# Optimization experiments

Measured on AMD Instinct MI355X. Metric: run time of the kernel, lower is better.

Reference implementation:

```python
import jax, jax.numpy as jnp
import numpy as np

N, E, B = 131072, 524288, 4096
NODES_PER_GRAPH = N // B  # 32


def setup_inputs() -> dict:
    key = jax.random.key(0)
    ks = jax.random.split(key, 16)
    def rn(k, shape, scale=0.05):
        return jax.random.normal(k, shape, jnp.float32) * scale
    return {
        "drug": jax.random.normal(ks[0], (N, 9), jnp.float32),
        "edge_index": jax.random.randint(ks[1], (2, E), 0, N),
        "batch_index": jnp.arange(N) // NODES_PER_GRAPH,  # sorted, every graph non-empty
        "protein": jax.random.normal(ks[2], (B, 1, 768), jnp.float32),
        # GCNConv layers (W: [in,out], b: [out])
        "gcn1_W": rn(ks[3], (9, 64)), "gcn1_b": jnp.zeros((64,), jnp.float32),
        "gcn2_W": rn(ks[4], (64, 64)), "gcn2_b": jnp.zeros((64,), jnp.float32),
        # GCN_output_layer Linear(128, 768)
        "out_W": rn(ks[5], (128, 768)), "out_b": jnp.zeros((768,), jnp.float32),
        # CNN_layers Conv1d stack
        "conv1_W": rn(ks[6], (32, 2, 3)), "conv1_b": jnp.zeros((32,), jnp.float32),
        "conv2_W": rn(ks[7], (32, 32, 3)), "conv2_b": jnp.zeros((32,), jnp.float32),
        "conv3_W": rn(ks[8], (32, 32, 3)), "conv3_b": jnp.zeros((32,), jnp.float32),
        # CBAM channel attention MLP (no bias): Linear(32,16), Linear(16,32)
        "ca_W1": rn(ks[9], (16, 32)), "ca_W2": rn(ks[10], (32, 16)),
        # SAM spatial conv Conv1d(2,1,3,pad=1)
        "sam_W": rn(ks[11], (1, 2, 3)), "sam_b": jnp.zeros((1,), jnp.float32),
        # CNN_linear MLP
        "lin1_W": rn(ks[12], (32, 12288)), "lin1_b": jnp.zeros((32,), jnp.float32),
        "lin2_W": rn(ks[13], (32, 32)), "lin2_b": jnp.zeros((32,), jnp.float32),
        "lin3_W": rn(ks[14], (1, 32)), "lin3_b": jnp.zeros((1,), jnp.float32),
    }


def gcn_conv(x, W, b, src, dst, n):
    """PyG GCNConv: self-loops + symmetric deg^-1/2 normalization."""
    h = x @ W  # [n, out]
    loop = jnp.arange(n)
    s = jnp.concatenate([src, loop])
    d = jnp.concatenate([dst, loop])
    deg = jax.ops.segment_sum(jnp.ones_like(d, x.dtype), d, num_segments=n)
    dinv = jax.lax.rsqrt(deg)  # deg >= 1 due to self-loops
    norm = dinv[s] * dinv[d]
    return jax.ops.segment_sum(h[s] * norm[:, None], d, num_segments=n) + b


def conv1d(x, w, b):
    y = jax.lax.conv_general_dilated(x, w, (1,), [(1, 1)],
                                     dimension_numbers=("NCH", "OIH", "NCH"))
    return y + b[None, :, None]


def reference(drug, edge_index, batch_index, protein,
              gcn1_W, gcn1_b, gcn2_W, gcn2_b, out_W, out_b,
              conv1_W, conv1_b, conv2_W, conv2_b, conv3_W, conv3_b,
              ca_W1, ca_W2, sam_W, sam_b,
              lin1_W, lin1_b, lin2_W, lin2_b, lin3_W, lin3_b):
    n = drug.shape[0]
    b_graphs = protein.shape[0]
    src, dst = edge_index[0], edge_index[1]

    x = jnp.tanh(gcn_conv(drug, gcn1_W, gcn1_b, src, dst, n))
    x = jnp.tanh(gcn_conv(x, gcn2_W, gcn2_b, src, dst, n))
    x = gcn_conv(x, gcn2_W, gcn2_b, src, dst, n)  # GCN2 reused, no activation

    gmax = jax.ops.segment_max(x, batch_index, num_segments=b_graphs)
    cnt = jax.ops.segment_sum(jnp.ones((n, 1), x.dtype), batch_index, num_segments=b_graphs)
    gmean = jax.ops.segment_sum(x, batch_index, num_segments=b_graphs) / cnt
    pooled = jnp.concatenate([gmax, gmean], axis=1)  # [B, 128]

    gcn_out = (pooled @ out_W + out_b)[:, None, :]  # [B, 1, 768]
    combined = jnp.concatenate([gcn_out, protein], axis=1)  # [B, 2, 768]

    h = conv1d(combined, conv1_W, conv1_b)
    h = conv1d(h, conv2_W, conv2_b)
    h = conv1d(h, conv3_W, conv3_b)  # [B, 32, 768]
    # dropout is identity at inference

    # CBAM: channel attention
    x1 = jnp.max(h, axis=-1)   # [B, 32]
    x2 = jnp.mean(h, axis=-1)  # [B, 32]
    mlp = lambda v: jax.nn.relu((v @ ca_W1.T) @ ca_W2.T)
    feats = jax.nn.sigmoid(mlp(x1) + mlp(x2))
    h = h * feats[:, :, None]
    # CBAM: spatial attention
    xm = jnp.mean(h, axis=1, keepdims=True)
    xM = jnp.max(h, axis=1, keepdims=True)
    att = jax.nn.sigmoid(conv1d(jnp.concatenate([xm, xM], axis=1), sam_W, sam_b))
    h = h * att

    # MaxPool1d(kernel_size=2)
    Bc, C, L = h.shape
    h = h.reshape(Bc, C, L // 2, 2).max(axis=-1)
    h = h.reshape(Bc, -1)  # [B, 12288]

    h = jax.nn.softplus(h @ lin1_W.T + lin1_b)
    h = jax.nn.softplus(h @ lin2_W.T + lin2_b)
    out = jax.nn.softplus(h @ lin3_W.T + lin3_b)
    return out
```

## Files before the change

### kernel.cpp

```cpp
#include <hip/hip_runtime.h>
#include <cstdint>
#include <cstddef>

#define NN 131072
#define EE 524288
#define BB 4096
#define LL 768

typedef __attribute__((ext_vector_type(8))) short bf16x8;
typedef __attribute__((ext_vector_type(4))) float f32x4;
typedef __attribute__((ext_vector_type(2))) unsigned int uint2v;

__device__ __forceinline__ float b2f(unsigned short u) {
  return __uint_as_float(((unsigned int)u) << 16);
}
__device__ __forceinline__ unsigned short f2b(float f) {
  unsigned int x = __float_as_uint(f);
  x += 0x7fff + ((x >> 16) & 1);
  return (unsigned short)(x >> 16);
}
__device__ __forceinline__ unsigned f2b2(float lo, float hi) {
#if __has_builtin(__builtin_amdgcn_cvt_pk_bf16_f32)
  typedef __attribute__((ext_vector_type(2))) __bf16 bf16v2;
  bf16v2 r = __builtin_amdgcn_cvt_pk_bf16_f32(lo, hi);
  return __builtin_bit_cast(unsigned, r);
#else
  return (unsigned)f2b(lo) | ((unsigned)f2b(hi) << 16);
#endif
}
__device__ __forceinline__ float sigm(float x) { return 1.f / (1.f + expf(-x)); }
__device__ __forceinline__ float softplus_(float x) {
  return fmaxf(x, 0.f) + log1pf(expf(-fabsf(x)));
}

__global__ __launch_bounds__(256) void k_zeroi(int* __restrict__ p) {
  p[blockIdx.x * 256 + threadIdx.x] = 0;
}
__global__ __launch_bounds__(256) void k_hist(const int* __restrict__ ei,
                                              int* __restrict__ degi) {
  int e = blockIdx.x * 256 + threadIdx.x;
  atomicAdd(&degi[ei[EE + e]], 1);
}
__global__ __launch_bounds__(256) void k_scan1(const int* __restrict__ degi,
                                               int* __restrict__ incl,
                                               int* __restrict__ bsum) {
  __shared__ int s[256];
  int t = threadIdx.x;
  int i = blockIdx.x * 256 + t;
  s[t] = degi[i];
  __syncthreads();
  for (int off = 1; off < 256; off <<= 1) {
    int u = (t >= off) ? s[t - off] : 0;
    __syncthreads();
    s[t] += u;
    __syncthreads();
  }
  incl[i] = s[t];
  if (t == 255) bsum[blockIdx.x] = s[t];
}
__global__ __launch_bounds__(512) void k_scan2(const int* __restrict__ bsum,
                                               int* __restrict__ bexcl) {
  __shared__ int s[512];
  int t = threadIdx.x;
  s[t] = bsum[t];
  __syncthreads();
  int orig = s[t];
  for (int off = 1; off < 512; off <<= 1) {
    int u = (t >= off) ? s[t - off] : 0;
    __syncthreads();
    s[t] += u;
    __syncthreads();
  }
  bexcl[t] = s[t] - orig;
}
__global__ __launch_bounds__(256) void k_scan3(const int* __restrict__ incl,
                                               const int* __restrict__ degi,
                                               const int* __restrict__ bexcl,
                                               int* __restrict__ offs,
                                               float* __restrict__ dinv) {
  int t = threadIdx.x;
  int i = blockIdx.x * 256 + t;
  offs[i] = incl[i] - degi[i] + bexcl[blockIdx.x];
  dinv[i] = rsqrtf((float)degi[i] + 1.0f);
  if (i == 0) offs[NN] = EE;
}
__global__ __launch_bounds__(256) void k_scatter(const int* __restrict__ ei,
                                                 const int* __restrict__ offs,
                                                 int* __restrict__ cur,
                                                 int* __restrict__ csr) {
  int e = blockIdx.x * 256 + threadIdx.x;
  int dst = ei[EE + e];
  int pos = atomicAdd(&cur[dst], 1);
  csr[offs[dst] + pos] = ei[e];
}

__global__ __launch_bounds__(256) void k_mm1(const float* __restrict__ drug,
                                             const float* __restrict__ W,
                                             const float* __restrict__ dinv,
                                             unsigned short* __restrict__ g) {
  __shared__ float Ws[9 * 64];
  int t = threadIdx.x;
  for (int i = t; i < 576; i += 256) Ws[i] = W[i];
  __syncthreads();
  int node = blockIdx.x * 4 + (t >> 6);
  int f = t & 63;
  const float* dr = drug + (size_t)node * 9;
  float s = 0.f;
#pragma unroll
  for (int k = 0; k < 9; k++) s += dr[k] * Ws[k * 64 + f];
  g[(size_t)node * 64 + f] = f2b(dinv[node] * s);
}

__global__ __launch_bounds__(256) void k_prepg(const float* __restrict__ W,
                                               unsigned short* __restrict__ Wgb) {
  int idx = blockIdx.x * 256 + threadIdx.x;
  int j = idx & 7;
  int lane = (idx >> 3) & 63;
  int nt = (idx >> 9) & 3;
  int kc = idx >> 11;
  int k = kc * 32 + (lane >> 4) * 8 + j;
  int o = nt * 16 + (lane & 15);
  Wgb[idx] = f2b(W[k * 64 + o]);
}

template <bool TANH>
__global__ __launch_bounds__(256) void k_layer(const unsigned short* __restrict__ gin,
                                               const int* __restrict__ offs,
                                               const int* __restrict__ csr,
                                               const float* __restrict__ dinv,
                                               const float* __restrict__ bias,
                                               const unsigned short* __restrict__ Wgb,
                                               unsigned short* __restrict__ outb) {
  __shared__ alignas(16) unsigned short xa[32 * 72];
  __shared__ alignas(16) float dis[32];
  const int t = threadIdx.x;
  const int wv = t >> 6, f = t & 63;
  const int lx = f & 15, quad = f >> 4;
  const int n0 = blockIdx.x * 32;
  const float bf = bias[f];
  for (int it = 0; it < 8; it++) {
    const int dl = wv * 8 + it;
    const int d = n0 + dl;
    const float di = dinv[d];
    const int j0 = offs[d], j1 = offs[d + 1];
    float acc = b2f(gin[(size_t)d * 64 + f]);
    int j = j0;
    for (; j + 4 <= j1; j += 4) {
      int s0 = csr[j], s1 = csr[j + 1], s2 = csr[j + 2], s3 = csr[j + 3];
      acc += (b2f(gin[(size_t)s0 * 64 + f]) + b2f(gin[(size_t)s1 * 64 + f]))
           + (b2f(gin[(size_t)s2 * 64 + f]) + b2f(gin[(size_t)s3 * 64 + f]));
    }
    for (; j < j1; j++) acc += b2f(gin[(size_t)csr[j] * 64 + f]);
    float v = di * acc + bf;
    if (TANH) v = tanhf(v);
    xa[dl * 72 + f] = f2b(v);
    if (f == 0) dis[dl] = di;
  }
  __syncthreads();
  const int mt = wv >> 1, np = wv & 1;
  bf16x8 A0 = *(const bf16x8*)&xa[(mt * 16 + lx) * 72 + quad * 8];
  bf16x8 A1 = *(const bf16x8*)&xa[(mt * 16 + lx) * 72 + 32 + quad * 8];
  f32x4 accs[2];
#pragma unroll
  for (int nn = 0; nn < 2; nn++) {
    int nt = np * 2 + nn;
    bf16x8 B0 = *(const bf16x8*)&Wgb[((0 * 4 + nt) * 64 + f) * 8];
    bf16x8 B1 = *(const bf16x8*)&Wgb[((1 * 4 + nt) * 64 + f) * 8];
    f32x4 acc = {0.f, 0.f, 0.f, 0.f};
    acc = __builtin_amdgcn_mfma_f32_16x16x32_bf16(A0, B0, acc, 0, 0, 0);
    acc = __builtin_amdgcn_mfma_f32_16x16x32_bf16(A1, B1, acc, 0, 0, 0);
    accs[nn] = acc;
  }
  f32x4 dq = *(const f32x4*)&dis[mt * 16 + quad * 4];
  __syncthreads();
#pragma unroll
  for (int nn = 0; nn < 2; nn++) {
    int nt = np * 2 + nn;
#pragma unroll
    for (int r = 0; r < 4; r++)
      xa[(mt * 16 + quad * 4 + r) * 72 + nt * 16 + lx] = f2b(dq[r] * accs[nn][r]);
  }
  __syncthreads();
  {
    int node = t >> 3, c8 = t & 7;
    *(f32x4*)(outb + (size_t)(n0 + node) * 64 + c8 * 8) =
        *(const f32x4*)(xa + node * 72 + c8 * 8);
  }
}

__global__ __launch_bounds__(512) void k_lastpool(const unsigned short* __restrict__ gin,
                                                  const int* __restrict__ offs,
                                                  const int* __restrict__ csr,
                                                  const float* __restrict__ dinv,
                                                  const float* __restrict__ bias,
                                                  float* __restrict__ pooled) {
  __shared__ float smax[8][64], ssum[8][64];
  const int t = threadIdx.x;
  const int f = t & 63, grp = t >> 6;
  const int g = blockIdx.x;
  const float bf = bias[f];
  float mx = -1e30f, sm = 0.f;
#pragma unroll
  for (int i = 0; i < 4; i++) {
    int d = g * 32 + grp * 4 + i;
    const float di = dinv[d];
    const int j0 = offs[d], j1 = offs[d + 1];
    float acc = b2f(gin[(size_t)d * 64 + f]);
    int j = j0;
    for (; j + 4 <= j1; j += 4) {
      int s0 = csr[j], s1 = csr[j + 1], s2 = csr[j + 2], s3 = csr[j + 3];
      acc += (b2f(gin[(size_t)s0 * 64 + f]) + b2f(gin[(size_t)s1 * 64 + f]))
           + (b2f(gin[(size_t)s2 * 64 + f]) + b2f(gin[(size_t)s3 * 64 + f]));
    }
    for (; j < j1; j++) acc += b2f(gin[(size_t)csr[j] * 64 + f]);
    float v = di * acc + bf;
    mx = fmaxf(mx, v);
    sm += v;
  }
  smax[grp][f] = mx;
  ssum[grp][f] = sm;
  __syncthreads();
  if (t < 64) {
    float m = smax[0][t], s = ssum[0][t];
#pragma unroll
    for (int w = 1; w < 8; w++) { m = fmaxf(m, smax[w][t]); s += ssum[w][t]; }
    pooled[(size_t)g * 128 + t] = m;
    pooled[(size_t)g * 128 + 64 + t] = s * (1.f / 32.f);
  }
}

__global__ __launch_bounds__(256) void k_outmm(const float* __restrict__ pooled,
                                               const float* __restrict__ W,
                                               const float* __restrict__ bias,
                                               unsigned short* __restrict__ gout) {
  __shared__ float ps[16][128];
  int t = threadIdx.x;
  int g0 = blockIdx.x * 16;
  for (int i = t; i < 16 * 128; i += 256) ps[i >> 7][i & 127] = pooled[(size_t)g0 * 128 + i];
  __syncthreads();
  float a0[16], a1[16], a2[16];
#pragma unroll
  for (int j = 0; j < 16; j++) { a0[j] = 0.f; a1[j] = 0.f; a2[j] = 0.f; }
  for (int k = 0; k < 128; k++) {
    float w0 = W[k * 768 + t];
    float w1 = W[k * 768 + t + 256];
    float w2 = W[k * 768 + t + 512];
#pragma unroll
    for (int j = 0; j < 16; j++) {
      float p = ps[j][k];
      a0[j] += p * w0; a1[j] += p * w1; a2[j] += p * w2;
    }
  }
  float b0 = bias[t], b1 = bias[t + 256], b2 = bias[t + 512];
  for (int j = 0; j < 16; j++) {
    gout[(size_t)(g0 + j) * 768 + t]       = f2b(a0[j] + b0);
    gout[(size_t)(g0 + j) * 768 + t + 256] = f2b(a1[j] + b1);
    gout[(size_t)(g0 + j) * 768 + t + 512] = f2b(a2[j] + b2);
  }
}

__global__ __launch_bounds__(512) void k_prepk7(
    const float* __restrict__ W1, const float* __restrict__ b1,
    const float* __restrict__ W2, const float* __restrict__ b2,
    const float* __restrict__ W3, const float* __restrict__ b3,
    unsigned short* __restrict__ Kcb, float* __restrict__ bconst) {
  __shared__ float W1s[192], W2s[3072], W3s[3072];
  __shared__ float b1s[32], b2s[32], b3s[32];
  __shared__ float M[320];
  __shared__ float beta[32];
  __shared__ float KcS[448];
  const int t = threadIdx.x;
  for (int i = t; i < 3072; i += 512) { W2s[i] = W2[i]; W3s[i] = W3[i]; }
  if (t < 192) W1s[t] = W1[t];
  if (t >= 192 && t < 224) { int i = t - 192; b1s[i] = b1[i]; b2s[i] = b2[i]; b3s[i] = b3[i]; }
  __syncthreads();
  if (t < 320) {
    int i = t / 10, rem = t % 10, c = rem / 5, t12 = rem % 5;
    float s = 0.f;
    for (int j = 0; j < 32; j++)
#pragma unroll
      for (int t2 = 0; t2 < 3; t2++) {
        int t1 = t12 - t2;
        if (t1 >= 0 && t1 < 3) s += W2s[(i * 32 + j) * 3 + t2] * W1s[(j * 2 + c) * 3 + t1];
      }
    M[i * 10 + c * 5 + t12] = s;
  }
  if (t >= 384 && t < 416) {
    int i = t - 384;
    float s = b2s[i];
    for (int j = 0; j < 32; j++) {
      float w = W2s[(i * 32 + j) * 3] + W2s[(i * 32 + j) * 3 + 1] + W2s[(i * 32 + j) * 3 + 2];
      s += w * b1s[j];
    }
    beta[i] = s;
  }
  __syncthreads();
  if (t < 448) {
    int o = t / 14, rem = t % 14, c = rem / 7, tt = rem % 7;
    float s = 0.f;
    for (int i = 0; i < 32; i++)
#pragma unroll
      for (int t3 = 0; t3 < 3; t3++) {
        int t12 = tt - t3;
        if (t12 >= 0 && t12 < 5) s += W3s[(o * 32 + i) * 3 + t3] * M[i * 10 + c * 5 + t12];
      }
    KcS[t] = s;
  }
  if (t >= 480 && t < 512) {
    int o = t - 480;
    float s = b3s[o];
    for (int i = 0; i < 32; i++) {
      float w = W3s[(o * 32 + i) * 3] + W3s[(o * 32 + i) * 3 + 1] + W3s[(o * 32 + i) * 3 + 2];
      s += w * beta[i];
    }
    bconst[o] = s;
  }
  __syncthreads();
  for (int i = t; i < 1024; i += 512) {
    int o = i >> 5, k = i & 31;
    Kcb[i] = (k < 14) ? f2b(KcS[o * 14 + k]) : (unsigned short)0;
  }
}

__global__ __launch_bounds__(64) void k_prepedge(
    const float* __restrict__ W1, const float* __restrict__ b1,
    const float* __restrict__ W2, const float* __restrict__ b2,
    const float* __restrict__ W3, const float* __restrict__ b3,
    float* __restrict__ edgeK, float* __restrict__ edgeB) {
  __shared__ float W1s[192], W2s[3072], W3s[3072];
  __shared__ float b1s[32], b2s[32], b3s[32];
  __shared__ float cl[2][6], h1[32][5], h2[32][4];
  const int t = threadIdx.x;
  const int side = blockIdx.x / 13, run = blockIdx.x % 13;
  for (int i = t; i < 3072; i += 64) { W2s[i] = W2[i]; W3s[i] = W3[i]; }
  for (int i = t; i < 192; i += 64) W1s[i] = W1[i];
  if (t < 32) { b1s[t] = b1[t]; b2s[t] = b2[t]; b3s[t] = b3[t]; }
  if (t < 12) cl[t / 6][t % 6] = (run == t) ? 1.f : 0.f;
  __syncthreads();
  const bool ub = (run == 12);
  if (t < 32) {
    int i = t;
    for (int p = 0; p < 5; p++) {
      float s = ub ? b1s[i] : 0.f;
      for (int c = 0; c < 2; c++)
#pragma unroll
        for (int tau = 0; tau < 3; tau++) {
          int x = (side == 0) ? (p + tau - 1) : (p + tau);
          if (x >= 0 && x < 6) s += W1s[(i * 2 + c) * 3 + tau] * cl[c][x];
        }
      h1[i][p] = s;
    }
  }
  __syncthreads();
  if (t < 32) {
    int o = t;
    for (int u = 0; u < 4; u++) {
      float s = ub ? b2s[o] : 0.f;
      for (int i = 0; i < 32; i++)
#pragma unroll
        for (int tau = 0; tau < 3; tau++) {
          int q = (side == 0) ? (u + tau - 1) : (u + tau);
          if (q >= 0 && q < 5) s += W2s[(o * 32 + i) * 3 + tau] * h1[i][q];
        }
      h2[o][u] = s;
    }
  }
  __syncthreads();
  if (t < 32) {
    int o = t;
    for (int e = 0; e < 2; e++) {
      float s = ub ? b3s[o] : 0.f;
      for (int i = 0; i < 32; i++)
#pragma unroll
        for (int tau = 0; tau < 3; tau++) {
          int u = (side == 0) ? (e + tau - 1) : (e + tau + 1);
          if (u >= 0 && u < 4) s += W3s[(o * 32 + i) * 3 + tau] * h2[i][u];
        }
      int slot = (side * 2 + e) * 32 + o;
      if (ub) edgeB[slot] = s;
      else edgeK[slot * 12 + run] = s;
    }
  }
}

__global__ __launch_bounds__(256) void k_prepw(const float* __restrict__ W,
                                               unsigned short* __restrict__ Wb) {
  int idx = blockIdx.x * 256 + threadIdx.x;
  int j = idx & 7;
  int lane = (idx >> 3) & 63;
  int nt = (idx >> 9) & 1;
  int kt = idx >> 10;
  int o = nt * 16 + (lane & 15);
  int k = kt * 32 + (lane >> 4) * 8 + j;
  int korig = (k & 31) * 384 + (k >> 5);
  Wb[idx] = f2b(W[(size_t)o * 12288 + korig]);
}

__global__ __launch_bounds__(512) void k_cnn(
    const unsigned short* __restrict__ gout, const float* __restrict__ protein,
    const unsigned short* __restrict__ Kcb, const float* __restrict__ bconst,
    const float* __restrict__ edgeK, const float* __restrict__ edgeB,
    const float* __restrict__ caW1, const float* __restrict__ caW2,
    const float* __restrict__ samW, const float* __restrict__ samb,
    unsigned short* __restrict__ pvec) {
  __shared__ float combf[2][776];
  __shared__ alignas(16) unsigned short im2[768 * 16];
  __shared__ float xbuf[2320];
  __shared__ float bcs[32];
  __shared__ float wmaxs[8][32], wsums[8][32];
  __shared__ float cmaxs[32], csums[32], t1buf[2][16], feats[32], samWs[8];
  const int t = threadIdx.x;
  const int b = blockIdx.x;
  const int lane = t & 63, wv = t >> 6, lx = lane & 15, quad = lane >> 4;

  for (int i = t; i < 1552; i += 512) {
    int c = i / 776, li = i - c * 776;
    int l = li - 4;
    float v = 0.f;
    if (l >= 0 && l < LL)
      v = c ? protein[(size_t)b * LL + l] : b2f(gout[(size_t)b * LL + l]);
    combf[c][li] = v;
  }
  if (t < 32) bcs[t] = bconst[t];
  if (t >= 32 && t < 38) samWs[t - 32] = samW[t - 32];
  if (t == 38) samWs[6] = samb[0];
  __syncthreads();

  for (int p = 0; p < 24; p++) {
    int idx = t + p * 512;
    int l = idx >> 4, k = idx & 15;
    unsigned short v = 0;
    if (k < 14) {
      int c = (k >= 7) ? 1 : 0;
      int q = k - c * 7;
      v = f2b(combf[c][l + 1 + q]);
    }
    im2[idx] = v;
  }
  __syncthreads();

  f32x4 a3[6][2];
  {
    bf16x8 A0 = *(const bf16x8*)&Kcb[(0 * 16 + lx) * 32 + quad * 8];
    bf16x8 A1 = *(const bf16x8*)&Kcb[(1 * 16 + lx) * 32 + quad * 8];
    f32x4 ci0, ci1;
#pragma unroll
    for (int r = 0; r < 4; r++) {
      ci0[r] = bcs[quad * 4 + r];
      ci1[r] = bcs[16 + quad * 4 + r];
    }
#pragma unroll
    for (int n = 0; n < 6; n++) {
      int l = (wv * 6 + n) * 16 + lx;
      bf16x8 Bf = {0, 0, 0, 0, 0, 0, 0, 0};
      if (quad < 2) Bf = *(const bf16x8*)&im2[l * 16 + quad * 8];
      a3[n][0] = __builtin_amdgcn_mfma_f32_16x16x32_bf16(A0, Bf, ci0, 0, 0, 0);
      a3[n][1] = __builtin_amdgcn_mfma_f32_16x16x32_bf16(A1, Bf, ci1, 0, 0, 0);
    }
  }
  {
    bool left = (wv == 0 && lx < 2);
    bool right = (wv == 7 && lx >= 14);
    if (left || right) {
      int n = left ? 0 : 5;
      int e = left ? lx : (lx - 14);
      int side = left ? 0 : 1;
      int cbase = left ? 4 : 766;
#pragma unroll
      for (int mt = 0; mt < 2; mt++)
#pragma unroll
        for (int r = 0; r < 4; r++) {
          int o = mt * 16 + quad * 4 + r;
          int slot = (side * 2 + e) * 32 + o;
          float s = edgeB[slot];
          const float* ek = &edgeK[slot * 12];
#pragma unroll
          for (int w = 0; w < 6; w++)
            s += ek[w] * combf[0][cbase + w] + ek[6 + w] * combf[1][cbase + w];
          a3[n][mt][r] = s;
        }
    }
  }

  float tmax[2][4], tsum[2][4];
#pragma unroll
  for (int mt = 0; mt < 2; mt++)
#pragma unroll
    for (int r = 0; r < 4; r++) { tmax[mt][r] = -1e30f; tsum[mt][r] = 0.f; }
#pragma unroll
  for (int n = 0; n < 6; n++)
#pragma unroll
    for (int mt = 0; mt < 2; mt++)
#pragma unroll
      for (int r = 0; r < 4; r++) {
        float v = a3[n][mt][r];
        tmax[mt][r] = fmaxf(tmax[mt][r], v);
        tsum[mt][r] += v;
      }
#pragma unroll
  for (int mt = 0; mt < 2; mt++)
#pragma unroll
    for (int r = 0; r < 4; r++) {
      float m = tmax[mt][r], s = tsum[mt][r];
      for (int d = 1; d < 16; d <<= 1) {
        m = fmaxf(m, __shfl_xor(m, d));
        s += __shfl_xor(s, d);
      }
      if (lx == 0) {
        wmaxs[wv][mt * 16 + quad * 4 + r] = m;
        wsums[wv][mt * 16 + quad * 4 + r] = s;
      }
    }
  __syncthreads();

  if (t < 32) {
    float m = wmaxs[0][t], s = wsums[0][t];
#pragma unroll
    for (int w = 1; w < 8; w++) { m = fmaxf(m, wmaxs[w][t]); s += wsums[w][t]; }
    cmaxs[t] = m;
    csums[t] = s;
  }
  __syncthreads();
  if (t < 32) {
    int j = t & 15;
    int mean = t >> 4;
    float s = 0.f;
    for (int o = 0; o < 32; o++) {
      float v = mean ? csums[o] * (1.f / 768.f) : cmaxs[o];
      s += v * caW1[j * 32 + o];
    }
    t1buf[mean][j] = s;
  }
  __syncthreads();
  if (t < 32) {
    float m1 = 0.f, m2 = 0.f;
    for (int j = 0; j < 16; j++) {
      m1 += t1buf[0][j] * caW2[t * 16 + j];
      m2 += t1buf[1][j] * caW2[t * 16 + j];
    }
    feats[t] = sigm(fmaxf(m1, 0.f) + fmaxf(m2, 0.f));
  }
  __syncthreads();

  float frq[2][4];
#pragma unroll
  for (int mt = 0; mt < 2; mt++)
#pragma unroll
    for (int r = 0; r < 4; r++) frq[mt][r] = feats[mt * 16 + quad * 4 + r];
#pragma unroll
  for (int n = 0; n < 6; n++) {
    int l = (wv * 6 + n) * 16 + lx;
    float sm = 0.f, mx = -1e30f;
#pragma unroll
    for (int mt = 0; mt < 2; mt++)
#pragma unroll
      for (int r = 0; r < 4; r++) {
        float v = a3[n][mt][r] * frq[mt][r];
        sm += v;
        mx = fmaxf(mx, v);
      }
    sm += __shfl_xor(sm, 16); mx = fmaxf(mx, __shfl_xor(mx, 16));
    sm += __shfl_xor(sm, 32); mx = fmaxf(mx, __shfl_xor(mx, 32));
    if (quad == 0) {
      xbuf[l] = sm * (1.f / 32.f);
      xbuf[772 + l] = mx;
    }
  }
  __syncthreads();

  for (int l = t; l < LL; l += 512) {
    float a = samWs[6];
#pragma unroll
    for (int k = 0; k < 3; k++) {
      int ll = l + k - 1;
      float vm = (ll >= 0 && ll < LL) ? xbuf[ll] : 0.f;
      float vM = (ll >= 0 && ll < LL) ? xbuf[772 + ll] : 0.f;
      a += samWs[k] * vm + samWs[3 + k] * vM;
    }
    xbuf[1544 + l] = sigm(a);
  }
  __syncthreads();

#pragma unroll
  for (int n = 0; n < 6; n++) {
    int l = (wv * 6 + n) * 16 + lx;
    float at = xbuf[1544 + l];
    float m[2][4];
#pragma unroll
    for (int mt = 0; mt < 2; mt++)
#pragma unroll
      for (int r = 0; r < 4; r++) {
        float v = a3[n][mt][r] * frq[mt][r] * at;
        m[mt][r] = fmaxf(v, __shfl_xor(v, 1));
      }
    if (!(lx & 1)) {
      int lp = l >> 1;
#pragma unroll
      for (int mt = 0; mt < 2; mt++) {
        uint2v pk;
        pk.x = f2b2(m[mt][0], m[mt][1]);
        pk.y = f2b2(m[mt][2], m[mt][3]);
        *(uint2v*)&pvec[(size_t)b * 12288 + lp * 32 + mt * 16 + quad * 4] = pk;
      }
    }
  }
}

__global__ __launch_bounds__(512) void k_mlp1(
    const unsigned short* __restrict__ pvec, const unsigned short* __restrict__ Wb,
    float* __restrict__ partial) {
  __shared__ float part[8][32][32];
  const int t = threadIdx.x;
  const int lane = t & 63, wv = t >> 6, lx = lane & 15, quad = lane >> 4;
  const int g0 = (blockIdx.x >> 2) * 32;
  const int kc = blockIdx.x & 3;
  const unsigned short* arow0 = pvec + (size_t)(g0 + lx) * 12288 + quad * 8;
  const unsigned short* arow1 = pvec + (size_t)(g0 + 16 + lx) * 12288 + quad * 8;

  f32x4 a00 = {0.f, 0.f, 0.f, 0.f}, a01 = a00, a10 = a00, a11 = a00;
  const int kt0 = kc * 96 + wv * 12;
#pragma unroll 4
  for (int i = 0; i < 12; i++) {
    const int kt = kt0 + i;
    bf16x8 A0 = *(const bf16x8*)&arow0[kt * 32];
    bf16x8 A1 = *(const bf16x8*)&arow1[kt * 32];
    bf16x8 B0 = *(const bf16x8*)&Wb[((kt * 2 + 0) * 64 + lane) * 8];
    bf16x8 B1 = *(const bf16x8*)&Wb[((kt * 2 + 1) * 64 + lane) * 8];
    a00 = __builtin_amdgcn_mfma_f32_16x16x32_bf16(A0, B0, a00, 0, 0, 0);
    a01 = __builtin_amdgcn_mfma_f32_16x16x32_bf16(A0, B1, a01, 0, 0, 0);
    a10 = __builtin_amdgcn_mfma_f32_16x16x32_bf16(A1, B0, a10, 0, 0, 0);
    a11 = __builtin_amdgcn_mfma_f32_16x16x32_bf16(A1, B1, a11, 0, 0, 0);
  }
#pragma unroll
  for (int r = 0; r < 4; r++) {
    part[wv][quad * 4 + r][lx]            = a00[r];
    part[wv][quad * 4 + r][16 + lx]       = a01[r];
    part[wv][16 + quad * 4 + r][lx]       = a10[r];
    part[wv][16 + quad * 4 + r][16 + lx]  = a11[r];
  }
  __syncthreads();
#pragma unroll
  for (int p = 0; p < 2; p++) {
    int idx = t + p * 512;
    int g = idx >> 5, o = idx & 31;
    float s = 0.f;
#pragma unroll
    for (int w = 0; w < 8; w++) s += part[w][g][o];
    partial[((size_t)kc * BB + g0 + g) * 32 + o] = s;
  }
}

__global__ __launch_bounds__(512) void k_mlp2(
    const float* __restrict__ partial,
    const float* __restrict__ lb1, const float* __restrict__ W2,
    const float* __restrict__ lb2, const float* __restrict__ W3,
    const float* __restrict__ lb3, float* __restrict__ out) {
  __shared__ float s1[16][32];
  __shared__ float s2[16][32];
  const int t = threadIdx.x;
  const int g0 = blockIdx.x * 16;
  {
    int g = t >> 5, o = t & 31;
    float s = lb1[o];
#pragma unroll
    for (int kc = 0; kc < 4; kc++) s += partial[((size_t)kc * BB + g0 + g) * 32 + o];
    s1[g][o] = softplus_(s);
  }
  __syncthreads();
  {
    int g = t >> 5, o = t & 31;
    float s = lb2[o];
    for (int kk = 0; kk < 32; kk++) s += s1[g][kk] * W2[o * 32 + kk];
    s2[g][o] = softplus_(s);
  }
  __syncthreads();
  if (t < 16) {
    float s = lb3[0];
    for (int kk = 0; kk < 32; kk++) s += s2[t][kk] * W3[kk];
    out[g0 + t] = softplus_(s);
  }
}

extern "C" void kernel_launch(void* const* d_in, const int* in_sizes, int n_in,
                              void* d_out, int out_size, void* d_ws, size_t ws_size,
                              hipStream_t stream) {
  const float* drug    = (const float*)d_in[0];
  const int*   ei      = (const int*)d_in[1];
  const float* protein = (const float*)d_in[3];
  const float* g1W = (const float*)d_in[4];
  const float* g1b = (const float*)d_in[5];
  const float* g2W = (const float*)d_in[6];
  const float* g2b = (const float*)d_in[7];
  const float* oW  = (const float*)d_in[8];
  const float* ob  = (const float*)d_in[9];
  const float* c1W = (const float*)d_in[10];
  const float* c1b = (const float*)d_in[11];
  const float* c2W = (const float*)d_in[12];
  const float* c2b = (const float*)d_in[13];
  const float* c3W = (const float*)d_in[14];
  const float* c3b = (const float*)d_in[15];
  const float* caW1 = (const float*)d_in[16];
  const float* caW2 = (const float*)d_in[17];
  const float* samW = (const float*)d_in[18];
  const float* samb = (const float*)d_in[19];
  const float* l1W = (const float*)d_in[20];
  const float* l1b = (const float*)d_in[21];
  const float* l2W = (const float*)d_in[22];
  const float* l2b = (const float*)d_in[23];
  const float* l3W = (const float*)d_in[24];
  const float* l3b = (const float*)d_in[25];

  char* ws = (char*)d_ws;
  float* dinv  = (float*)(ws);
  int*   degi  = (int*)(ws + (size_t)524288);
  int*   cur   = (int*)(ws + (size_t)1048576);
  int*   offs  = (int*)(ws + (size_t)1572864);
  int*   bsum  = (int*)(ws + (size_t)2621440);
  int*   bexcl = (int*)(ws + (size_t)2625536);
  int*   csr   = (int*)(ws + (size_t)3145728);
  unsigned short* gA = (unsigned short*)(ws + (size_t)5242880);
  unsigned short* gB = (unsigned short*)(ws + (size_t)22020096);
  unsigned short* pvec = (unsigned short*)(ws + (size_t)5242880);
  float* pooled = (float*)(ws + (size_t)105906176);
  unsigned short* gout = (unsigned short*)(ws + (size_t)108003328);
  unsigned short* Wb   = (unsigned short*)(ws + (size_t)114294784);
  float* bconst  = (float*)(ws + (size_t)115083136);
  float* edgeK   = (float*)(ws + (size_t)115083264);
  float* edgeB   = (float*)(ws + (size_t)115089408);
  unsigned short* Kcb = (unsigned short*)(ws + (size_t)115090432);
  unsigned short* Wgb = (unsigned short*)(ws + (size_t)115092480);
  float* partial = (float*)(ws + (size_t)115343360);
  float* outp = (float*)d_out;

  k_zeroi<<<2 * NN / 256, 256, 0, stream>>>(degi);
  k_hist<<<EE / 256, 256, 0, stream>>>(ei, degi);
  k_scan1<<<NN / 256, 256, 0, stream>>>(degi, offs, bsum);
  k_scan2<<<1, 512, 0, stream>>>(bsum, bexcl);
  k_scan3<<<NN / 256, 256, 0, stream>>>(offs, degi, bexcl, offs, dinv);
  k_scatter<<<EE / 256, 256, 0, stream>>>(ei, offs, cur, csr);
  k_prepw<<<(12288 * 32) / 256, 256, 0, stream>>>(l1W, Wb);
  k_prepg<<<16, 256, 0, stream>>>(g2W, Wgb);
  k_prepk7<<<1, 512, 0, stream>>>(c1W, c1b, c2W, c2b, c3W, c3b, Kcb, bconst);
  k_prepedge<<<26, 64, 0, stream>>>(c1W, c1b, c2W, c2b, c3W, c3b, edgeK, edgeB);

  k_mm1<<<NN / 4, 256, 0, stream>>>(drug, g1W, dinv, gA);
  k_layer<true><<<NN / 32, 256, 0, stream>>>(gA, offs, csr, dinv, g1b, Wgb, gB);
  k_layer<true><<<NN / 32, 256, 0, stream>>>(gB, offs, csr, dinv, g2b, Wgb, gA);
  k_lastpool<<<BB, 512, 0, stream>>>(gA, offs, csr, dinv, g2b, pooled);

  k_outmm<<<BB / 16, 256, 0, stream>>>(pooled, oW, ob, gout);

  k_cnn<<<BB, 512, 0, stream>>>(gout, protein, Kcb, bconst, edgeK, edgeB,
                                caW1, caW2, samW, samb, pvec);

  k_mlp1<<<(BB / 32) * 4, 512, 0, stream>>>(pvec, Wb, partial);
  k_mlp2<<<BB / 16, 512, 0, stream>>>(partial, l1b, l2W, l2b, l3W, l3b, outp);
}
```

Before: 581.2 us.

## Make CNN kernel persistent over 16 graphs with prefetch; widen GCN layer blocks

k_cnn now runs 256 blocks, and each block loops over 16 graphs. It prefetches the next graph's gout/protein row into registers while the current graph is processed, and builds the im2col buffer with packed 16-byte bf16 stores instead of scalar stores. The xbuf scratch is folded into combf plus a smaller attention buffer. Separately, the GCN layer kernels go to 512 threads covering 64 nodes per block. The aim is to cut launch and block-setup overhead and hide global load latency. The risk is that one block per CU with a serial chain of syncs leaves too little parallelism to hide latency.

```diff
diff --git a/kernel.cpp b/kernel.cpp
--- a/kernel.cpp
+++ b/kernel.cpp
@@ -10,6 +10,7 @@
 typedef __attribute__((ext_vector_type(8))) short bf16x8;
 typedef __attribute__((ext_vector_type(4))) float f32x4;
 typedef __attribute__((ext_vector_type(2))) unsigned int uint2v;
+typedef __attribute__((ext_vector_type(4))) unsigned int uint4v;
 
 __device__ __forceinline__ float b2f(unsigned short u) {
   return __uint_as_float(((unsigned int)u) << 16);
@@ -124,19 +125,19 @@
 }
 
 template <bool TANH>
-__global__ __launch_bounds__(256) void k_layer(const unsigned short* __restrict__ gin,
+__global__ __launch_bounds__(512) void k_layer(const unsigned short* __restrict__ gin,
                                                const int* __restrict__ offs,
                                                const int* __restrict__ csr,
                                                const float* __restrict__ dinv,
                                                const float* __restrict__ bias,
                                                const unsigned short* __restrict__ Wgb,
                                                unsigned short* __restrict__ outb) {
-  __shared__ alignas(16) unsigned short xa[32 * 72];
-  __shared__ alignas(16) float dis[32];
+  __shared__ alignas(16) unsigned short xa[64 * 72];
+  __shared__ alignas(16) float dis[64];
   const int t = threadIdx.x;
   const int wv = t >> 6, f = t & 63;
   const int lx = f & 15, quad = f >> 4;
-  const int n0 = blockIdx.x * 32;
+  const int n0 = blockIdx.x * 64;
   const float bf = bias[f];
   for (int it = 0; it < 8; it++) {
     const int dl = wv * 8 + it;
@@ -403,52 +404,88 @@
     const float* __restrict__ caW1, const float* __restrict__ caW2,
     const float* __restrict__ samW, const float* __restrict__ samb,
     unsigned short* __restrict__ pvec) {
-  __shared__ float combf[2][776];
+  __shared__ float combf[1552];
   __shared__ alignas(16) unsigned short im2[768 * 16];
-  __shared__ float xbuf[2320];
+  __shared__ float attb[768];
   __shared__ float bcs[32];
   __shared__ float wmaxs[8][32], wsums[8][32];
   __shared__ float cmaxs[32], csums[32], t1buf[2][16], feats[32], samWs[8];
   const int t = threadIdx.x;
-  const int b = blockIdx.x;
   const int lane = t & 63, wv = t >> 6, lx = lane & 15, quad = lane >> 4;
-
-  for (int i = t; i < 1552; i += 512) {
-    int c = i / 776, li = i - c * 776;
-    int l = li - 4;
-    float v = 0.f;
-    if (l >= 0 && l < LL)
-      v = c ? protein[(size_t)b * LL + l] : b2f(gout[(size_t)b * LL + l]);
-    combf[c][li] = v;
-  }
+  const int bstart = blockIdx.x * 16;
+
   if (t < 32) bcs[t] = bconst[t];
   if (t >= 32 && t < 38) samWs[t - 32] = samW[t - 32];
   if (t == 38) samWs[6] = samb[0];
   __syncthreads();
-
-  for (int p = 0; p < 24; p++) {
-    int idx = t + p * 512;
-    int l = idx >> 4, k = idx & 15;
-    unsigned short v = 0;
-    if (k < 14) {
-      int c = (k >= 7) ? 1 : 0;
-      int q = k - c * 7;
-      v = f2b(combf[c][l + 1 + q]);
-    }
-    im2[idx] = v;
-  }
-  __syncthreads();
-
-  f32x4 a3[6][2];
-  {
-    bf16x8 A0 = *(const bf16x8*)&Kcb[(0 * 16 + lx) * 32 + quad * 8];
-    bf16x8 A1 = *(const bf16x8*)&Kcb[(1 * 16 + lx) * 32 + quad * 8];
-    f32x4 ci0, ci1;
-#pragma unroll
-    for (int r = 0; r < 4; r++) {
-      ci0[r] = bcs[quad * 4 + r];
-      ci1[r] = bcs[16 + quad * 4 + r];
-    }
+  bf16x8 A0 = *(const bf16x8*)&Kcb[(0 * 16 + lx) * 32 + quad * 8];
+  bf16x8 A1 = *(const bf16x8*)&Kcb[(1 * 16 + lx) * 32 + quad * 8];
+  f32x4 ci0, ci1;
+#pragma unroll
+  for (int r = 0; r < 4; r++) {
+    ci0[r] = bcs[quad * 4 + r];
+    ci1[r] = bcs[16 + quad * 4 + r];
+  }
+
+  float rv[3];
+#pragma unroll
+  for (int j = 0; j < 3; j++) {
+    int i = t + j * 512;
+    float v = 0.f;
+    if (i < 1552) {
+      int c = (i >= 776) ? 1 : 0;
+      int l = i - c * 776 - 4;
+      if (l >= 0 && l < LL)
+        v = c ? protein[(size_t)bstart * LL + l] : b2f(gout[(size_t)bstart * LL + l]);
+    }
+    rv[j] = v;
+  }
+
+  for (int gs = 0; gs < 16; gs++) {
+    const int b = bstart + gs;
+#pragma unroll
+    for (int j = 0; j < 3; j++) {
+      int i = t + j * 512;
+      if (i < 1552) combf[i] = rv[j];
+    }
+    __syncthreads();
+    {
+      const int gp = (b + 1 < BB) ? b + 1 : b;
+#pragma unroll
+      for (int j = 0; j < 3; j++) {
+        int i = t + j * 512;
+        float v = 0.f;
+        if (i < 1552) {
+          int c = (i >= 776) ? 1 : 0;
+          int l = i - c * 776 - 4;
+          if (l >= 0 && l < LL)
+            v = c ? protein[(size_t)gp * LL + l] : b2f(gout[(size_t)gp * LL + l]);
+        }
+        rv[j] = v;
+      }
+    }
+
+    for (int p = 0; p < 3; p++) {
+      int idx = t + p * 512;
+      int l = idx >> 1, half = idx & 1;
+      uint4v pk;
+      if (half == 0) {
+        float v0 = combf[l + 1], v1 = combf[l + 2], v2 = combf[l + 3], v3 = combf[l + 4];
+        float v4 = combf[l + 5], v5 = combf[l + 6], v6 = combf[l + 7];
+        float v7 = combf[776 + l + 1];
+        pk[0] = f2b2(v0, v1); pk[1] = f2b2(v2, v3);
+        pk[2] = f2b2(v4, v5); pk[3] = f2b2(v6, v7);
+      } else {
+        float v0 = combf[776 + l + 2], v1 = combf[776 + l + 3], v2 = combf[776 + l + 4];
+        float v3 = combf[776 + l + 5], v4 = combf[776 + l + 6], v5 = combf[776 + l + 7];
+        pk[0] = f2b2(v0, v1); pk[1] = f2b2(v2, v3);
+        pk[2] = f2b2(v4, v5); pk[3] = 0u;
+      }
+      *(uint4v*)&im2[l * 16 + half * 8] = pk;
+    }
+    __syncthreads();
+
+    f32x4 a3[6][2];
 #pragma unroll
     for (int n = 0; n < 6; n++) {
       int l = (wv * 6 + n) * 16 + lx;
@@ -457,152 +494,155 @@
       a3[n][0] = __builtin_amdgcn_mfma_f32_16x16x32_bf16(A0, Bf, ci0, 0, 0, 0);
       a3[n][1] = __builtin_amdgcn_mfma_f32_16x16x32_bf16(A1, Bf, ci1, 0, 0, 0);
     }
-  }
-  {
-    bool left = (wv == 0 && lx < 2);
-    bool right = (wv == 7 && lx >= 14);
-    if (left || right) {
-      int n = left ? 0 : 5;
-      int e = left ? lx : (lx - 14);
-      int side = left ? 0 : 1;
-      int cbase = left ? 4 : 766;
+    {
+      bool left = (wv == 0 && lx < 2);
+      bool right = (wv == 7 && lx >= 14);
+      if (left || right) {
+        int n = left ? 0 : 5;
+        int e = left ? lx : (lx - 14);
+        int side = left ? 0 : 1;
+        int cbase = left ? 4 : 766;
+#pragma unroll
+        for (int mt = 0; mt < 2; mt++)
+#pragma unroll
+          for (int r = 0; r < 4; r++) {
+            int o = mt * 16 + quad * 4 + r;
+            int slot = (side * 2 + e) * 32 + o;
+            float s = edgeB[slot];
+            const float* ek = &edgeK[slot * 12];
+#pragma unroll
+            for (int w = 0; w < 6; w++)
+              s += ek[w] * combf[cbase + w] + ek[6 + w] * combf[776 + cbase + w];
+            a3[n][mt][r] = s;
+          }
+      }
+    }
+
+    float tmax[2][4], tsum[2][4];
+#pragma unroll
+    for (int mt = 0; mt < 2; mt++)
+#pragma unroll
+      for (int r = 0; r < 4; r++) { tmax[mt][r] = -1e30f; tsum[mt][r] = 0.f; }
+#pragma unroll
+    for (int n = 0; n < 6; n++)
 #pragma unroll
       for (int mt = 0; mt < 2; mt++)
 #pragma unroll
         for (int r = 0; r < 4; r++) {
-          int o = mt * 16 + quad * 4 + r;
-          int slot = (side * 2 + e) * 32 + o;
-          float s = edgeB[slot];
-          const float* ek = &edgeK[slot * 12];
-#pragma unroll
-          for (int w = 0; w < 6; w++)
-            s += ek[w] * combf[0][cbase + w] + ek[6 + w] * combf[1][cbase + w];
-          a3[n][mt][r] = s;
-        }
-    }
-  }
-
-  float tmax[2][4], tsum[2][4];
-#pragma unroll
-  for (int mt = 0; mt < 2; mt++)
-#pragma unroll
-    for (int r = 0; r < 4; r++) { tmax[mt][r] = -1e30f; tsum[mt][r] = 0.f; }
-#pragma unroll
-  for (int n = 0; n < 6; n++)
+          float v = a3[n][mt][r];
+          tmax[mt][r] = fmaxf(tmax[mt][r], v);
+          tsum[mt][r] += v;
+        }
 #pragma unroll
     for (int mt = 0; mt < 2; mt++)
 #pragma unroll
       for (int r = 0; r < 4; r++) {
-        float v = a3[n][mt][r];
-        tmax[mt][r] = fmaxf(tmax[mt][r], v);
-        tsum[mt][r] += v;
-      }
-#pragma unroll
-  for (int mt = 0; mt < 2; mt++)
-#pragma unroll
-    for (int r = 0; r < 4; r++) {
-      float m = tmax[mt][r], s = tsum[mt][r];
-      for (int d = 1; d < 16; d <<= 1) {
-        m = fmaxf(m, __shfl_xor(m, d));
-        s += __shfl_xor(s, d);
-      }
-      if (lx == 0) {
-        wmaxs[wv][mt * 16 + quad * 4 + r] = m;
-        wsums[wv][mt * 16 + quad * 4 + r] = s;
-      }
-    }
-  __syncthreads();
-
-  if (t < 32) {
-    float m = wmaxs[0][t], s = wsums[0][t];
-#pragma unroll
-    for (int w = 1; w < 8; w++) { m = fmaxf(m, wmaxs[w][t]); s += wsums[w][t]; }
-    cmaxs[t] = m;
-    csums[t] = s;
-  }
-  __syncthreads();
-  if (t < 32) {
-    int j = t & 15;
-    int mean = t >> 4;
-    float s = 0.f;
-    for (int o = 0; o < 32; o++) {
-      float v = mean ? csums[o] * (1.f / 768.f) : cmaxs[o];
-      s += v * caW1[j * 32 + o];
-    }
-    t1buf[mean][j] = s;
-  }
-  __syncthreads();
-  if (t < 32) {
-    float m1 = 0.f, m2 = 0.f;
-    for (int j = 0; j < 16; j++) {
-      m1 += t1buf[0][j] * caW2[t * 16 + j];
-      m2 += t1buf[1][j] * caW2[t * 16 + j];
-    }
-    feats[t] = sigm(fmaxf(m1, 0.f) + fmaxf(m2, 0.f));
-  }
-  __syncthreads();
-
-  float frq[2][4];
-#pragma unroll
-  for (int mt = 0; mt < 2; mt++)
-#pragma unroll
-    for (int r = 0; r < 4; r++) frq[mt][r] = feats[mt * 16 + quad * 4 + r];
-#pragma unroll
-  for (int n = 0; n < 6; n++) {
-    int l = (wv * 6 + n) * 16 + lx;
-    float sm = 0.f, mx = -1e30f;
+        float m = tmax[mt][r], s = tsum[mt][r];
+        for (int d = 1; d < 16; d <<= 1) {
+          m = fmaxf(m, __shfl_xor(m, d));
+          s += __shfl_xor(s, d);
+        }
+        if (lx == 0) {
+          wmaxs[wv][mt * 16 + quad * 4 + r] = m;
+          wsums[wv][mt * 16 + quad * 4 + r] = s;
+        }
+      }
+    __syncthreads();
+
+    if (t < 32) {
+      float m = wmaxs[0][t], s = wsums[0][t];
+#pragma unroll
+      for (int w = 1; w < 8; w++) { m = fmaxf(m, wmaxs[w][t]); s += wsums[w][t]; }
+      cmaxs[t] = m;
+      csums[t] = s;
+    }
+    __syncthreads();
+    if (t < 32) {
+      int j = t & 15;
+      int mean = t >> 4;
+      float s = 0.f;
+      for (int o = 0; o < 32; o++) {
+        float v = mean ? csums[o] * (1.f / 768.f) : cmaxs[o];
+        s += v * caW1[j * 32 + o];
+      }
+      t1buf[mean][j] = s;
+    }
+    __syncthreads();
+    if (t < 32) {
+      float m1 = 0.f, m2 = 0.f;
+      for (int j = 0; j < 16; j++) {
+        m1 += t1buf[0][j] * caW2[t * 16 + j];
+        m2 += t1buf[1][j] * caW2[t * 16 + j];
+      }
+      feats[t] = sigm(fmaxf(m1, 0.f) + fmaxf(m2, 0.f));
+    }
+    __syncthreads();
+
+    float* xmb = combf;
+    float* xMb = combf + 772;
+    float frq[2][4];
 #pragma unroll
     for (int mt = 0; mt < 2; mt++)
 #pragma unroll
-      for (int r = 0; r < 4; r++) {
-        float v = a3[n][mt][r] * frq[mt][r];
-        sm += v;
-        mx = fmaxf(mx, v);
-      }
-    sm += __shfl_xor(sm, 16); mx = fmaxf(mx, __shfl_xor(mx, 16));
-    sm += __shfl_xor(sm, 32); mx = fmaxf(mx, __shfl_xor(mx, 32));
-    if (quad == 0) {
-      xbuf[l] = sm * (1.f / 32.f);
-      xbuf[772 + l] = mx;
-    }
-  }
-  __syncthreads();
-
-  for (int l = t; l < LL; l += 512) {
-    float a = samWs[6];
-#pragma unroll
-    for (int k = 0; k < 3; k++) {
-      int ll = l + k - 1;
-      float vm = (ll >= 0 && ll < LL) ? xbuf[ll] : 0.f;
-      float vM = (ll >= 0 && ll < LL) ? xbuf[772 + ll] : 0.f;
-      a += samWs[k] * vm + samWs[3 + k] * vM;
-    }
-    xbuf[1544 + l] = sigm(a);
-  }
-  __syncthreads();
-
-#pragma unroll
-  for (int n = 0; n < 6; n++) {
-    int l = (wv * 6 + n) * 16 + lx;
-    float at = xbuf[1544 + l];
-    float m[2][4];
-#pragma unroll
-    for (int mt = 0; mt < 2; mt++)
-#pragma unroll
-      for (int r = 0; r < 4; r++) {
-        float v = a3[n][mt][r] * frq[mt][r] * at;
-        m[mt][r] = fmaxf(v, __shfl_xor(v, 1));
-      }
-    if (!(lx & 1)) {
-      int lp = l >> 1;
-#pragma unroll
-      for (int mt = 0; mt < 2; mt++) {
-        uint2v pk;
-        pk.x = f2b2(m[mt][0], m[mt][1]);
-        pk.y = f2b2(m[mt][2], m[mt][3]);
-        *(uint2v*)&pvec[(size_t)b * 12288 + lp * 32 + mt * 16 + quad * 4] = pk;
-      }
-    }
+      for (int r = 0; r < 4; r++) frq[mt][r] = feats[mt * 16 + quad * 4 + r];
+#pragma unroll
+    for (int n = 0; n < 6; n++) {
+      int l = (wv * 6 + n) * 16 + lx;
+      float sm = 0.f, mx = -1e30f;
+#pragma unroll
+      for (int mt = 0; mt < 2; mt++)
+#pragma unroll
+        for (int r = 0; r < 4; r++) {
+          float v = a3[n][mt][r] * frq[mt][r];
+          sm += v;
+          mx = fmaxf(mx, v);
+        }
+      sm += __shfl_xor(sm, 16); mx = fmaxf(mx, __shfl_xor(mx, 16));
+      sm += __shfl_xor(sm, 32); mx = fmaxf(mx, __shfl_xor(mx, 32));
+      if (quad == 0) {
+        xmb[l] = sm * (1.f / 32.f);
+        xMb[l] = mx;
+      }
+    }
+    __syncthreads();
+
+    for (int l = t; l < LL; l += 512) {
+      float a = samWs[6];
+#pragma unroll
+      for (int k = 0; k < 3; k++) {
+        int ll = l + k - 1;
+        float vm = (ll >= 0 && ll < LL) ? xmb[ll] : 0.f;
+        float vM = (ll >= 0 && ll < LL) ? xMb[ll] : 0.f;
+        a += samWs[k] * vm + samWs[3 + k] * vM;
+      }
+      attb[l] = sigm(a);
+    }
+    __syncthreads();
+
+#pragma unroll
+    for (int n = 0; n < 6; n++) {
+      int l = (wv * 6 + n) * 16 + lx;
+      float at = attb[l];
+      float m[2][4];
+#pragma unroll
+      for (int mt = 0; mt < 2; mt++)
+#pragma unroll
+        for (int r = 0; r < 4; r++) {
+          float v = a3[n][mt][r] * frq[mt][r] * at;
+          m[mt][r] = fmaxf(v, __shfl_xor(v, 1));
+        }
+      if (!(lx & 1)) {
+        int lp = l >> 1;
+#pragma unroll
+        for (int mt = 0; mt < 2; mt++) {
+          uint2v pk;
+          pk.x = f2b2(m[mt][0], m[mt][1]);
+          pk.y = f2b2(m[mt][2], m[mt][3]);
+          *(uint2v*)&pvec[(size_t)b * 12288 + lp * 32 + mt * 16 + quad * 4] = pk;
+        }
+      }
+    }
+    __syncthreads();
   }
 }
 
@@ -744,14 +784,14 @@
   k_prepedge<<<26, 64, 0, stream>>>(c1W, c1b, c2W, c2b, c3W, c3b, edgeK, edgeB);
 
   k_mm1<<<NN / 4, 256, 0, stream>>>(drug, g1W, dinv, gA);
-  k_layer<true><<<NN / 32, 256, 0, stream>>>(gA, offs, csr, dinv, g1b, Wgb, gB);
-  k_layer<true><<<NN / 32, 256, 0, stream>>>(gB, offs, csr, dinv, g2b, Wgb, gA);
+  k_layer<true><<<NN / 64, 512, 0, stream>>>(gA, offs, csr, dinv, g1b, Wgb, gB);
+  k_layer<true><<<NN / 64, 512, 0, stream>>>(gB, offs, csr, dinv, g2b, Wgb, gA);
   k_lastpool<<<BB, 512, 0, stream>>>(gA, offs, csr, dinv, g2b, pooled);
 
   k_outmm<<<BB / 16, 256, 0, stream>>>(pooled, oW, ob, gout);
 
-  k_cnn<<<BB, 512, 0, stream>>>(gout, protein, Kcb, bconst, edgeK, edgeB,
-                                caW1, caW2, samW, samb, pvec);
+  k_cnn<<<BB / 16, 512, 0, stream>>>(gout, protein, Kcb, bconst, edgeK, edgeB,
+                                     caW1, caW2, samW, samb, pvec);
 
   k_mlp1<<<(BB / 32) * 4, 512, 0, stream>>>(pvec, Wb, partial);
   k_mlp2<<<BB / 16, 512, 0, stream>>>(partial, l1b, l2W, l2b, l3W, l3b, outp);
```

After: 548.3 us. 5.7% less time.
